# Performance work log

Hardware: AMD Instinct MI355X
Metric: run time of the kernel (lower is better)

## Reference

```python
import jax, jax.numpy as jnp
import numpy as np

B, S, H, I = 2, 1024, 1024, 4096
G, E = 4, 4
NE = G * E
CAP = 1024


def setup_inputs() -> dict:
    key = jax.random.key(0)
    ks = jax.random.split(key, 6)
    return {
        "hidden_states": jax.random.normal(ks[0], (B, S, H), jnp.float32),
        "group_router_w": jax.random.normal(ks[1], (G, H), jnp.float32) * 0.02,
        "expert_router_w": jax.random.normal(ks[2], (G, E, H), jnp.float32) * 0.02,
        "gate_w": jax.random.normal(ks[3], (NE, I, H), jnp.float32) * 0.02,
        "up_w": jax.random.normal(ks[4], (NE, I, H), jnp.float32) * 0.02,
        "down_w": jax.random.normal(ks[5], (NE, H, I), jnp.float32) * 0.02,
    }


def _forward(x, gw, erw, Wg, Wu, Wd):
    b, s, h = x.shape
    T = b * s
    xf = x.reshape(T, h)
    # level 1: group routing (fp32 softmax, top-2 groups)
    group_logits = xf @ gw.T                                        # [T,G]
    group_probs = jax.nn.softmax(group_logits.astype(jnp.float32), axis=-1)
    top_gp, top_gi = jax.lax.top_k(group_probs, 2)                  # [T,2]
    # level 2: per-group expert routing (top-1 expert within group)
    expert_logits = jnp.einsum('th,geh->tge', xf, erw)              # [T,G,E]
    expert_probs = jax.nn.softmax(expert_logits.astype(jnp.float32), axis=-1)
    e_idx = jnp.argmax(expert_probs, axis=-1)                       # [T,G]
    e_prob = jnp.max(expert_probs, axis=-1)                         # [T,G]
    sel_e = jnp.take_along_axis(e_idx, top_gi, axis=1)              # [T,2]
    sel_p = jnp.take_along_axis(e_prob, top_gi, axis=1)             # [T,2]
    eid = (top_gi * E + sel_e).reshape(-1)                          # [2T] global expert id
    wgt = (top_gp * sel_p).reshape(-1)                              # [2T] combine weight
    x2 = jnp.repeat(xf, 2, axis=0)                                  # [2T,H], slot-major per token
    # capacity-based dispatch: position within expert via cumsum of one-hot
    onehot = jax.nn.one_hot(eid, NE, dtype=jnp.int32)               # [2T,NE]
    pos = (jnp.cumsum(onehot, axis=0) * onehot).sum(axis=1) - 1     # [2T]
    keep = pos < CAP
    pos_c = jnp.where(keep, pos, CAP)                               # overflow -> dummy slot
    buf = jnp.zeros((NE, CAP + 1, h), x.dtype).at[eid, pos_c].set(x2)
    # grouped-GEMM gated FFN (SwiGLU) over all experts at once
    gate = jax.nn.silu(jnp.einsum('ech,eih->eci', buf, Wg))
    up = jnp.einsum('ech,eih->eci', buf, Wu)
    yexp = jnp.einsum('eci,ehi->ech', gate * up, Wd)                # [NE,CAP+1,H]
    # combine: gather back and weight; dropped tokens get zero weight
    y = yexp[eid, pos_c] * jnp.where(keep, wgt, 0.0)[:, None].astype(x.dtype)
    out = (y[0::2] + y[1::2]).reshape(b, s, h)
    aux_loss = jnp.zeros((), jnp.float32)  # aux-loss accumulation truncated in source; initialized to 0
    return out, aux_loss


def reference(hidden_states, group_router_w, expert_router_w, gate_w, up_w, down_w):
    return _forward(hidden_states, group_router_w, expert_router_w, gate_w, up_w, down_w)
```

## Files before the change

kernel.cpp:

```cpp
#include <hip/hip_runtime.h>
#include <hip/hip_bf16.h>

typedef float f32x4 __attribute__((ext_vector_type(4)));
typedef __bf16 bf16x8 __attribute__((ext_vector_type(8)));

#define H 1024
#define II 4096
#define NE 16
#define CAP 1024
#define NTOK 2048
#define NSLOT 4096

__global__ __launch_bounds__(256) void k_route(
    const float* __restrict__ x, const float* __restrict__ gw,
    const float* __restrict__ erw, int* __restrict__ eid,
    float* __restrict__ wgt) {
  int t = blockIdx.x * 4 + (threadIdx.x >> 6);
  int lane = threadIdx.x & 63;
  const float* xr = x + (size_t)t * H;
  double acc[20];
#pragma unroll
  for (int j = 0; j < 20; j++) acc[j] = 0.0;
  for (int it = 0; it < 16; ++it) {
    int h = it * 64 + lane;
    float xv = xr[h];
#pragma unroll
    for (int g = 0; g < 4; ++g) acc[g] += (double)xv * (double)gw[g * H + h];
#pragma unroll
    for (int j = 0; j < 16; ++j)
      acc[4 + j] += (double)xv * (double)erw[j * H + h];
  }
#pragma unroll
  for (int j = 0; j < 20; ++j) {
    double v = acc[j];
#pragma unroll
    for (int o = 32; o > 0; o >>= 1) v += __shfl_down(v, o, 64);
    acc[j] = v;
  }
  if (lane == 0) {
    float gl[4];
#pragma unroll
    for (int g = 0; g < 4; g++) gl[g] = (float)acc[g];
    int g1 = 0;
#pragma unroll
    for (int g = 1; g < 4; g++)
      if (gl[g] > gl[g1]) g1 = g;
    int g2 = (g1 == 0) ? 1 : 0;
#pragma unroll
    for (int g = 0; g < 4; g++)
      if (g != g1 && gl[g] > gl[g2]) g2 = g;
    float gm = fmaxf(fmaxf(gl[0], gl[1]), fmaxf(gl[2], gl[3]));
    float s = 0.f;
#pragma unroll
    for (int g = 0; g < 4; g++) s += expf(gl[g] - gm);
    float p[2] = {expf(gl[g1] - gm) / s, expf(gl[g2] - gm) / s};
    int gs[2] = {g1, g2};
#pragma unroll
    for (int k = 0; k < 2; k++) {
      int g = gs[k];
      float el[4];
#pragma unroll
      for (int e2 = 0; e2 < 4; e2++) el[e2] = (float)acc[4 + g * 4 + e2];
      int eb = 0;
#pragma unroll
      for (int e2 = 1; e2 < 4; e2++)
        if (el[e2] > el[eb]) eb = e2;
      float es = 0.f;
#pragma unroll
      for (int e2 = 0; e2 < 4; e2++) es += expf(el[e2] - el[eb]);
      eid[2 * t + k] = g * 4 + eb;
      wgt[2 * t + k] = p[k] * (1.f / es);
    }
  }
}

__global__ __launch_bounds__(1024) void k_scan(const int* __restrict__ eid,
                                               int* __restrict__ perm,
                                               int* __restrict__ cnt,
                                               int* __restrict__ kept) {
  int wid = threadIdx.x >> 6;
  int lane = threadIdx.x & 63;
  int base = 0;
  for (int it = 0; it < 64; ++it) {
    int slot = it * 64 + lane;
    int e = eid[slot];
    unsigned long long m = __ballot(e == wid);
    if (e == wid) {
      int pos = base + __popcll(m & ((1ull << lane) - 1ull));
      if (pos < CAP) {
        perm[wid * CAP + pos] = slot;
        kept[slot] = 1;
      } else {
        kept[slot] = 0;
      }
    }
    base += __popcll(m);
  }
  if (lane == 0) cnt[wid] = (base < CAP) ? base : CAP;
}

__global__ __launch_bounds__(256) void k_cvtx(const float* __restrict__ x,
                                              __bf16* __restrict__ xb) {
  size_t i = ((size_t)blockIdx.x * 256 + threadIdx.x) * 8;
  f32x4 a = *(const f32x4*)(x + i);
  f32x4 b = *(const f32x4*)(x + i + 4);
  bf16x8 o;
#pragma unroll
  for (int j = 0; j < 4; j++) {
    o[j] = (__bf16)a[j];
    o[j + 4] = (__bf16)b[j];
  }
  *(bf16x8*)(xb + i) = o;
}

__global__ __launch_bounds__(256) void k_gateup(
    const __bf16* __restrict__ xb, const float* __restrict__ Wg,
    const float* __restrict__ Wu, const int* __restrict__ perm,
    const int* __restrict__ cnt, __bf16* __restrict__ act) {
  __shared__ __bf16 As[2][128 * 64];
  __shared__ __bf16 Gs[2][64 * 64];
  __shared__ __bf16 Us[2][64 * 64];
  __shared__ int slotArr[128];
  const int e = blockIdx.z, nt = blockIdx.x, rt = blockIdx.y;
  const int ce = cnt[e];
  if (rt * 128 >= ce) return;
  const int tid = threadIdx.x, lane = tid & 63, wid = tid >> 6;
  if (tid < 128) {
    int ridx = rt * 128 + tid;
    slotArr[tid] = perm[e * CAP + (ridx < ce ? ridx : 0)];
  }
  __syncthreads();
  const int srow = tid >> 3;
  const int sch = tid & 7;
  const __bf16* pA[4];
  int wrA[4];
#pragma unroll
  for (int q = 0; q < 4; q++) {
    int r = q * 32 + srow;
    pA[q] = xb + (size_t)(slotArr[r] >> 1) * H + sch * 8;
    wrA[q] = r * 64 + (sch ^ (r & 7)) * 8;
  }
  const size_t ew = (size_t)e * II * H + (size_t)(nt * 64) * H;
  const float* pG[2];
  const float* pU[2];
  int wrW[2];
#pragma unroll
  for (int q = 0; q < 2; q++) {
    int r = q * 32 + srow;
    pG[q] = Wg + ew + (size_t)r * H + sch * 8;
    pU[q] = Wu + ew + (size_t)r * H + sch * 8;
    wrW[q] = r * 64 + (sch ^ (r & 7)) * 8;
  }
  const int wm = wid >> 1, wn = wid & 1;
  f32x4 accG[4][2], accU[4][2];
#pragma unroll
  for (int m = 0; m < 4; m++)
#pragma unroll
    for (int n = 0; n < 2; n++)
#pragma unroll
      for (int i = 0; i < 4; i++) {
        accG[m][n][i] = 0.f;
        accU[m][n][i] = 0.f;
      }
  {
    bf16x8 va[4];
    f32x4 g0[2], g1[2], u0[2], u1[2];
#pragma unroll
    for (int q = 0; q < 4; q++) va[q] = *(const bf16x8*)(pA[q]);
#pragma unroll
    for (int q = 0; q < 2; q++) {
      g0[q] = *(const f32x4*)(pG[q]);
      g1[q] = *(const f32x4*)(pG[q] + 4);
      u0[q] = *(const f32x4*)(pU[q]);
      u1[q] = *(const f32x4*)(pU[q] + 4);
    }
#pragma unroll
    for (int q = 0; q < 4; q++) *(bf16x8*)&As[0][wrA[q]] = va[q];
#pragma unroll
    for (int q = 0; q < 2; q++) {
      bf16x8 fg, fu;
#pragma unroll
      for (int i = 0; i < 4; i++) {
        fg[i] = (__bf16)g0[q][i];
        fg[i + 4] = (__bf16)g1[q][i];
        fu[i] = (__bf16)u0[q][i];
        fu[i + 4] = (__bf16)u1[q][i];
      }
      *(bf16x8*)&Gs[0][wrW[q]] = fg;
      *(bf16x8*)&Us[0][wrW[q]] = fu;
    }
  }
  __syncthreads();
  for (int t = 0; t < 16; ++t) {
    const int cb = t & 1, nb = cb ^ 1;
    bf16x8 va[4];
    f32x4 g0[2], g1[2], u0[2], u1[2];
    if (t < 15) {
      const int ko = (t + 1) * 64;
#pragma unroll
      for (int q = 0; q < 4; q++) va[q] = *(const bf16x8*)(pA[q] + ko);
#pragma unroll
      for (int q = 0; q < 2; q++) {
        g0[q] = *(const f32x4*)(pG[q] + ko);
        g1[q] = *(const f32x4*)(pG[q] + ko + 4);
        u0[q] = *(const f32x4*)(pU[q] + ko);
        u1[q] = *(const f32x4*)(pU[q] + ko + 4);
      }
    }
#pragma unroll
    for (int kk = 0; kk < 2; ++kk) {
      bf16x8 aF[4], gF[2], uF[2];
#pragma unroll
      for (int m = 0; m < 4; m++) {
        int r = wm * 64 + m * 16 + (lane & 15);
        int c = (kk * 4 + (lane >> 4)) ^ (r & 7);
        aF[m] = *(const bf16x8*)&As[cb][r * 64 + c * 8];
      }
#pragma unroll
      for (int n = 0; n < 2; n++) {
        int rg = wn * 32 + n * 16 + (lane & 15);
        int c = (kk * 4 + (lane >> 4)) ^ (rg & 7);
        gF[n] = *(const bf16x8*)&Gs[cb][rg * 64 + c * 8];
        uF[n] = *(const bf16x8*)&Us[cb][rg * 64 + c * 8];
      }
#pragma unroll
      for (int m = 0; m < 4; m++)
#pragma unroll
        for (int n = 0; n < 2; n++) {
          accG[m][n] = __builtin_amdgcn_mfma_f32_16x16x32_bf16(
              aF[m], gF[n], accG[m][n], 0, 0, 0);
          accU[m][n] = __builtin_amdgcn_mfma_f32_16x16x32_bf16(
              aF[m], uF[n], accU[m][n], 0, 0, 0);
        }
    }
    if (t < 15) {
#pragma unroll
      for (int q = 0; q < 4; q++) *(bf16x8*)&As[nb][wrA[q]] = va[q];
#pragma unroll
      for (int q = 0; q < 2; q++) {
        bf16x8 fg, fu;
#pragma unroll
        for (int i = 0; i < 4; i++) {
          fg[i] = (__bf16)g0[q][i];
          fg[i + 4] = (__bf16)g1[q][i];
          fu[i] = (__bf16)u0[q][i];
          fu[i + 4] = (__bf16)u1[q][i];
        }
        *(bf16x8*)&Gs[nb][wrW[q]] = fg;
        *(bf16x8*)&Us[nb][wrW[q]] = fu;
      }
    }
    __syncthreads();
  }
  const int colB = nt * 64 + wn * 32;
#pragma unroll
  for (int m = 0; m < 4; m++)
#pragma unroll
    for (int n = 0; n < 2; n++)
#pragma unroll
      for (int i = 0; i < 4; i++) {
        int row = wm * 64 + m * 16 + (lane >> 4) * 4 + i;
        if (rt * 128 + row < ce) {
          int slot = slotArr[row];
          float g = accG[m][n][i];
          float u = accU[m][n][i];
          float a = (g / (1.f + __expf(-g))) * u;
          act[(size_t)slot * II + colB + n * 16 + (lane & 15)] = (__bf16)a;
        }
      }
}

__global__ __launch_bounds__(256) void k_down(
    const __bf16* __restrict__ act, const float* __restrict__ Wd,
    const int* __restrict__ perm, const int* __restrict__ cnt,
    const float* __restrict__ wgt, float* __restrict__ y) {
  __shared__ __bf16 As[2][128 * 64];
  __shared__ __bf16 Ws[2][128 * 64];
  __shared__ int slotArr[128];
  const int e = blockIdx.z, nt = blockIdx.x, rt = blockIdx.y;
  const int ce = cnt[e];
  if (rt * 128 >= ce) return;
  const int tid = threadIdx.x, lane = tid & 63, wid = tid >> 6;
  if (tid < 128) {
    int ridx = rt * 128 + tid;
    slotArr[tid] = perm[e * CAP + (ridx < ce ? ridx : 0)];
  }
  __syncthreads();
  const int srow = tid >> 3;
  const int sch = tid & 7;
  const __bf16* pA[4];
  const float* pW[4];
  int wrA[4];
#pragma unroll
  for (int q = 0; q < 4; q++) {
    int r = q * 32 + srow;
    pA[q] = act + (size_t)slotArr[r] * II + sch * 8;
    pW[q] = Wd + (size_t)e * H * II + (size_t)(nt * 128 + r) * II + sch * 8;
    wrA[q] = r * 64 + (sch ^ (r & 7)) * 8;
  }
  const int wm = wid >> 1, wn = wid & 1;
  f32x4 acc[4][4];
#pragma unroll
  for (int m = 0; m < 4; m++)
#pragma unroll
    for (int n = 0; n < 4; n++)
#pragma unroll
      for (int i = 0; i < 4; i++) acc[m][n][i] = 0.f;
  {
    bf16x8 va[4];
    f32x4 w0[4], w1[4];
#pragma unroll
    for (int q = 0; q < 4; q++) {
      va[q] = *(const bf16x8*)(pA[q]);
      w0[q] = *(const f32x4*)(pW[q]);
      w1[q] = *(const f32x4*)(pW[q] + 4);
    }
#pragma unroll
    for (int q = 0; q < 4; q++) {
      *(bf16x8*)&As[0][wrA[q]] = va[q];
      bf16x8 fw;
#pragma unroll
      for (int i = 0; i < 4; i++) {
        fw[i] = (__bf16)w0[q][i];
        fw[i + 4] = (__bf16)w1[q][i];
      }
      *(bf16x8*)&Ws[0][wrA[q]] = fw;
    }
  }
  __syncthreads();
  for (int t = 0; t < 64; ++t) {
    const int cb = t & 1, nb = cb ^ 1;
    bf16x8 va[4];
    f32x4 w0[4], w1[4];
    if (t < 63) {
      const int ko = (t + 1) * 64;
#pragma unroll
      for (int q = 0; q < 4; q++) {
        va[q] = *(const bf16x8*)(pA[q] + ko);
        w0[q] = *(const f32x4*)(pW[q] + ko);
        w1[q] = *(const f32x4*)(pW[q] + ko + 4);
      }
    }
#pragma unroll
    for (int kk = 0; kk < 2; ++kk) {
      bf16x8 aF[4], wF[4];
#pragma unroll
      for (int m = 0; m < 4; m++) {
        int r = wm * 64 + m * 16 + (lane & 15);
        int c = (kk * 4 + (lane >> 4)) ^ (r & 7);
        aF[m] = *(const bf16x8*)&As[cb][r * 64 + c * 8];
      }
#pragma unroll
      for (int n = 0; n < 4; n++) {
        int rw = wn * 64 + n * 16 + (lane & 15);
        int c = (kk * 4 + (lane >> 4)) ^ (rw & 7);
        wF[n] = *(const bf16x8*)&Ws[cb][rw * 64 + c * 8];
      }
#pragma unroll
      for (int m = 0; m < 4; m++)
#pragma unroll
        for (int n = 0; n < 4; n++)
          acc[m][n] = __builtin_amdgcn_mfma_f32_16x16x32_bf16(aF[m], wF[n],
                                                              acc[m][n], 0, 0, 0);
    }
    if (t < 63) {
#pragma unroll
      for (int q = 0; q < 4; q++) {
        *(bf16x8*)&As[nb][wrA[q]] = va[q];
        bf16x8 fw;
#pragma unroll
        for (int i = 0; i < 4; i++) {
          fw[i] = (__bf16)w0[q][i];
          fw[i + 4] = (__bf16)w1[q][i];
        }
        *(bf16x8*)&Ws[nb][wrA[q]] = fw;
      }
    }
    __syncthreads();
  }
  const int colB = nt * 128 + wn * 64;
#pragma unroll
  for (int m = 0; m < 4; m++)
#pragma unroll
    for (int n = 0; n < 4; n++)
#pragma unroll
      for (int i = 0; i < 4; i++) {
        int row = wm * 64 + m * 16 + (lane >> 4) * 4 + i;
        if (rt * 128 + row < ce) {
          int slot = slotArr[row];
          y[(size_t)slot * H + colB + n * 16 + (lane & 15)] =
              wgt[slot] * acc[m][n][i];
        }
      }
}

__global__ __launch_bounds__(256) void k_combine(const float* __restrict__ y,
                                                 const int* __restrict__ kept,
                                                 float* __restrict__ out) {
  int t = blockIdx.x, tid = threadIdx.x;
  const f32x4* y0 = (const f32x4*)(y + (size_t)(2 * t) * H);
  const f32x4* y1 = (const f32x4*)(y + (size_t)(2 * t + 1) * H);
  f32x4 a, b;
#pragma unroll
  for (int i = 0; i < 4; i++) {
    a[i] = 0.f;
    b[i] = 0.f;
  }
  if (kept[2 * t]) a = y0[tid];
  if (kept[2 * t + 1]) b = y1[tid];
  ((f32x4*)out)[(size_t)t * 256 + tid] = a + b;
  if (t == 0 && tid == 0) out[(size_t)NTOK * H] = 0.f;
}

extern "C" void kernel_launch(void* const* d_in, const int* in_sizes, int n_in,
                              void* d_out, int out_size, void* d_ws,
                              size_t ws_size, hipStream_t stream) {
  const float* x = (const float*)d_in[0];
  const float* gw = (const float*)d_in[1];
  const float* erw = (const float*)d_in[2];
  const float* Wg = (const float*)d_in[3];
  const float* Wu = (const float*)d_in[4];
  const float* Wd = (const float*)d_in[5];
  float* out = (float*)d_out;
  char* ws = (char*)d_ws;
  int* eid = (int*)(ws);
  float* wgt = (float*)(ws + (16 << 10));
  int* kept = (int*)(ws + (32 << 10));
  int* cnt = (int*)(ws + (48 << 10));
  int* perm = (int*)(ws + (64 << 10));
  __bf16* act = (__bf16*)(ws + (128 << 10));
  float* yb = (float*)(ws + (128 << 10) + (size_t)NSLOT * II * 2);
  __bf16* xb = (__bf16*)(ws + (128 << 10) + (size_t)NSLOT * II * 2 +
                         (size_t)NSLOT * H * 4);

  k_route<<<NTOK / 4, 256, 0, stream>>>(x, gw, erw, eid, wgt);
  k_scan<<<1, 1024, 0, stream>>>(eid, perm, cnt, kept);
  k_cvtx<<<NTOK * H / 8 / 256, 256, 0, stream>>>(x, xb);
  k_gateup<<<dim3(64, 8, 16), 256, 0, stream>>>(xb, Wg, Wu, perm, cnt, act);
  k_down<<<dim3(8, 8, 16), 256, 0, stream>>>(act, Wd, perm, cnt, wgt, yb);
  k_combine<<<NTOK, 256, 0, stream>>>(yb, kept, out);
}
```

Before: 376.7 us.

## Deepen global prefetch to two stages and shrink down-proj N tile

Both grouped-GEMM kernels now keep two K-tiles of global loads in flight using ping-pong register sets. Each LDS buffer swap uses a custom lgkmcnt-wait plus barrier instead of __syncthreads. k_down's N tile is halved to 64 columns and its grid doubled, which adds blocks and cuts per-block LDS and accumulators. Both kernels get launch_bounds min-blocks 2 to raise occupancy. The risks are register pressure from the doubled prefetch registers and more redundant activation reads in k_down.

After: 372.5 us. Within noise of the previous version (-1.1%).

```diff
diff --git a/kernel.cpp b/kernel.cpp
--- a/kernel.cpp
+++ b/kernel.cpp
@@ -113,7 +113,12 @@
   *(bf16x8*)(xb + i) = o;
 }
 
-__global__ __launch_bounds__(256) void k_gateup(
+#define FENCE_BAR()                                    \
+  asm volatile("s_waitcnt lgkmcnt(0)" ::: "memory");   \
+  __builtin_amdgcn_sched_barrier(0);                   \
+  __builtin_amdgcn_s_barrier();
+
+__global__ __launch_bounds__(256, 2) void k_gateup(
     const __bf16* __restrict__ xb, const float* __restrict__ Wg,
     const float* __restrict__ Wu, const int* __restrict__ perm,
     const int* __restrict__ cnt, __bf16* __restrict__ act) {
@@ -162,95 +167,80 @@
         accG[m][n][i] = 0.f;
         accU[m][n][i] = 0.f;
       }
-  {
-    bf16x8 va[4];
-    f32x4 g0[2], g1[2], u0[2], u1[2];
-#pragma unroll
-    for (int q = 0; q < 4; q++) va[q] = *(const bf16x8*)(pA[q]);
-#pragma unroll
-    for (int q = 0; q < 2; q++) {
-      g0[q] = *(const f32x4*)(pG[q]);
-      g1[q] = *(const f32x4*)(pG[q] + 4);
-      u0[q] = *(const f32x4*)(pU[q]);
-      u1[q] = *(const f32x4*)(pU[q] + 4);
+  bf16x8 a0[4], a1[4];
+  f32x4 g00[2], g01[2], u00[2], u01[2];
+  f32x4 g10[2], g11[2], u10[2], u11[2];
+
+#define GU_LOADS(AS, G0, G1, U0, U1, T)                                    \
+  {                                                                        \
+    const int ko = (T) * 64;                                               \
+    _Pragma("unroll") for (int q = 0; q < 4; q++)                          \
+        AS[q] = *(const bf16x8*)(pA[q] + ko);                              \
+    _Pragma("unroll") for (int q = 0; q < 2; q++) {                        \
+      G0[q] = *(const f32x4*)(pG[q] + ko);                                 \
+      G1[q] = *(const f32x4*)(pG[q] + ko + 4);                             \
+      U0[q] = *(const f32x4*)(pU[q] + ko);                                 \
+      U1[q] = *(const f32x4*)(pU[q] + ko + 4);                             \
+    }                                                                      \
+  }
+#define GU_WRITE(BUF, AS, G0, G1, U0, U1)                                  \
+  {                                                                        \
+    _Pragma("unroll") for (int q = 0; q < 4; q++)                          \
+        *(bf16x8*)&As[BUF][wrA[q]] = AS[q];                                \
+    _Pragma("unroll") for (int q = 0; q < 2; q++) {                        \
+      bf16x8 fg, fu;                                                       \
+      _Pragma("unroll") for (int i = 0; i < 4; i++) {                      \
+        fg[i] = (__bf16)G0[q][i];                                          \
+        fg[i + 4] = (__bf16)G1[q][i];                                      \
+        fu[i] = (__bf16)U0[q][i];                                          \
+        fu[i + 4] = (__bf16)U1[q][i];                                      \
+      }                                                                    \
+      *(bf16x8*)&Gs[BUF][wrW[q]] = fg;                                     \
+      *(bf16x8*)&Us[BUF][wrW[q]] = fu;                                     \
+    }                                                                      \
+  }
+#define GU_COMPUTE(BUF)                                                    \
+  {                                                                        \
+    _Pragma("unroll") for (int kk = 0; kk < 2; ++kk) {                     \
+      bf16x8 aF[4], gF[2], uF[2];                                          \
+      _Pragma("unroll") for (int m = 0; m < 4; m++) {                      \
+        int r = wm * 64 + m * 16 + (lane & 15);                            \
+        int c = (kk * 4 + (lane >> 4)) ^ (r & 7);                          \
+        aF[m] = *(const bf16x8*)&As[BUF][r * 64 + c * 8];                  \
+      }                                                                    \
+      _Pragma("unroll") for (int n = 0; n < 2; n++) {                      \
+        int rg = wn * 32 + n * 16 + (lane & 15);                           \
+        int c = (kk * 4 + (lane >> 4)) ^ (rg & 7);                         \
+        gF[n] = *(const bf16x8*)&Gs[BUF][rg * 64 + c * 8];                 \
+        uF[n] = *(const bf16x8*)&Us[BUF][rg * 64 + c * 8];                 \
+      }                                                                    \
+      _Pragma("unroll") for (int m = 0; m < 4; m++)                        \
+          _Pragma("unroll") for (int n = 0; n < 2; n++) {                  \
+        accG[m][n] = __builtin_amdgcn_mfma_f32_16x16x32_bf16(              \
+            aF[m], gF[n], accG[m][n], 0, 0, 0);                            \
+        accU[m][n] = __builtin_amdgcn_mfma_f32_16x16x32_bf16(              \
+            aF[m], uF[n], accU[m][n], 0, 0, 0);                            \
+      }                                                                    \
+    }                                                                      \
+  }
+
+  GU_LOADS(a0, g00, g01, u00, u01, 0);
+  GU_LOADS(a1, g10, g11, u10, u11, 1);
+  GU_WRITE(0, a0, g00, g01, u00, u01);
+  FENCE_BAR();
+  for (int tt = 0; tt < 8; ++tt) {
+    const int t0 = 2 * tt;
+    if (t0 + 2 < 16) GU_LOADS(a0, g00, g01, u00, u01, t0 + 2);
+    GU_COMPUTE(0);
+    GU_WRITE(1, a1, g10, g11, u10, u11);
+    FENCE_BAR();
+    const int t1 = t0 + 1;
+    if (t1 + 2 < 16) GU_LOADS(a1, g10, g11, u10, u11, t1 + 2);
+    GU_COMPUTE(1);
+    if (t1 + 1 < 16) {
+      GU_WRITE(0, a0, g00, g01, u00, u01);
+      FENCE_BAR();
     }
-#pragma unroll
-    for (int q = 0; q < 4; q++) *(bf16x8*)&As[0][wrA[q]] = va[q];
-#pragma unroll
-    for (int q = 0; q < 2; q++) {
-      bf16x8 fg, fu;
-#pragma unroll
-      for (int i = 0; i < 4; i++) {
-        fg[i] = (__bf16)g0[q][i];
-        fg[i + 4] = (__bf16)g1[q][i];
-        fu[i] = (__bf16)u0[q][i];
-        fu[i + 4] = (__bf16)u1[q][i];
-      }
-      *(bf16x8*)&Gs[0][wrW[q]] = fg;
-      *(bf16x8*)&Us[0][wrW[q]] = fu;
-    }
-  }
-  __syncthreads();
-  for (int t = 0; t < 16; ++t) {
-    const int cb = t & 1, nb = cb ^ 1;
-    bf16x8 va[4];
-    f32x4 g0[2], g1[2], u0[2], u1[2];
-    if (t < 15) {
-      const int ko = (t + 1) * 64;
-#pragma unroll
-      for (int q = 0; q < 4; q++) va[q] = *(const bf16x8*)(pA[q] + ko);
-#pragma unroll
-      for (int q = 0; q < 2; q++) {
-        g0[q] = *(const f32x4*)(pG[q] + ko);
-        g1[q] = *(const f32x4*)(pG[q] + ko + 4);
-        u0[q] = *(const f32x4*)(pU[q] + ko);
-        u1[q] = *(const f32x4*)(pU[q] + ko + 4);
-      }
-    }
-#pragma unroll
-    for (int kk = 0; kk < 2; ++kk) {
-      bf16x8 aF[4], gF[2], uF[2];
-#pragma unroll
-      for (int m = 0; m < 4; m++) {
-        int r = wm * 64 + m * 16 + (lane & 15);
-        int c = (kk * 4 + (lane >> 4)) ^ (r & 7);
-        aF[m] = *(const bf16x8*)&As[cb][r * 64 + c * 8];
-      }
-#pragma unroll
-      for (int n = 0; n < 2; n++) {
-        int rg = wn * 32 + n * 16 + (lane & 15);
-        int c = (kk * 4 + (lane >> 4)) ^ (rg & 7);
-        gF[n] = *(const bf16x8*)&Gs[cb][rg * 64 + c * 8];
-        uF[n] = *(const bf16x8*)&Us[cb][rg * 64 + c * 8];
-      }
-#pragma unroll
-      for (int m = 0; m < 4; m++)
-#pragma unroll
-        for (int n = 0; n < 2; n++) {
-          accG[m][n] = __builtin_amdgcn_mfma_f32_16x16x32_bf16(
-              aF[m], gF[n], accG[m][n], 0, 0, 0);
-          accU[m][n] = __builtin_amdgcn_mfma_f32_16x16x32_bf16(
-              aF[m], uF[n], accU[m][n], 0, 0, 0);
-        }
-    }
-    if (t < 15) {
-#pragma unroll
-      for (int q = 0; q < 4; q++) *(bf16x8*)&As[nb][wrA[q]] = va[q];
-#pragma unroll
-      for (int q = 0; q < 2; q++) {
-        bf16x8 fg, fu;
-#pragma unroll
-        for (int i = 0; i < 4; i++) {
-          fg[i] = (__bf16)g0[q][i];
-          fg[i + 4] = (__bf16)g1[q][i];
-          fu[i] = (__bf16)u0[q][i];
-          fu[i + 4] = (__bf16)u1[q][i];
-        }
-        *(bf16x8*)&Gs[nb][wrW[q]] = fg;
-        *(bf16x8*)&Us[nb][wrW[q]] = fu;
-      }
-    }
-    __syncthreads();
   }
   const int colB = nt * 64 + wn * 32;
 #pragma unroll
@@ -270,12 +260,12 @@
       }
 }
 
-__global__ __launch_bounds__(256) void k_down(
+__global__ __launch_bounds__(256, 2) void k_down(
     const __bf16* __restrict__ act, const float* __restrict__ Wd,
     const int* __restrict__ perm, const int* __restrict__ cnt,
     const float* __restrict__ wgt, float* __restrict__ y) {
   __shared__ __bf16 As[2][128 * 64];
-  __shared__ __bf16 Ws[2][128 * 64];
+  __shared__ __bf16 Ws[2][64 * 64];
   __shared__ int slotArr[128];
   const int e = blockIdx.z, nt = blockIdx.x, rt = blockIdx.y;
   const int ce = cnt[e];
@@ -289,100 +279,99 @@
   const int srow = tid >> 3;
   const int sch = tid & 7;
   const __bf16* pA[4];
-  const float* pW[4];
   int wrA[4];
 #pragma unroll
   for (int q = 0; q < 4; q++) {
     int r = q * 32 + srow;
     pA[q] = act + (size_t)slotArr[r] * II + sch * 8;
-    pW[q] = Wd + (size_t)e * H * II + (size_t)(nt * 128 + r) * II + sch * 8;
     wrA[q] = r * 64 + (sch ^ (r & 7)) * 8;
   }
+  const float* pW[2];
+  int wrW[2];
+#pragma unroll
+  for (int q = 0; q < 2; q++) {
+    int r = q * 32 + srow;
+    pW[q] = Wd + (size_t)e * H * II + (size_t)(nt * 64 + r) * II + sch * 8;
+    wrW[q] = r * 64 + (sch ^ (r & 7)) * 8;
+  }
   const int wm = wid >> 1, wn = wid & 1;
-  f32x4 acc[4][4];
+  f32x4 acc[4][2];
 #pragma unroll
   for (int m = 0; m < 4; m++)
 #pragma unroll
-    for (int n = 0; n < 4; n++)
+    for (int n = 0; n < 2; n++)
 #pragma unroll
       for (int i = 0; i < 4; i++) acc[m][n][i] = 0.f;
-  {
-    bf16x8 va[4];
-    f32x4 w0[4], w1[4];
-#pragma unroll
-    for (int q = 0; q < 4; q++) {
-      va[q] = *(const bf16x8*)(pA[q]);
-      w0[q] = *(const f32x4*)(pW[q]);
-      w1[q] = *(const f32x4*)(pW[q] + 4);
+  bf16x8 a0[4], a1[4];
+  f32x4 w00[2], w01[2], w10[2], w11[2];
+
+#define DN_LOADS(AS, W0, W1, T)                                            \
+  {                                                                        \
+    const int ko = (T) * 64;                                               \
+    _Pragma("unroll") for (int q = 0; q < 4; q++)                          \
+        AS[q] = *(const bf16x8*)(pA[q] + ko);                              \
+    _Pragma("unroll") for (int q = 0; q < 2; q++) {                        \
+      W0[q] = *(const f32x4*)(pW[q] + ko);                                 \
+      W1[q] = *(const f32x4*)(pW[q] + ko + 4);                             \
+    }                                                                      \
+  }
+#define DN_WRITE(BUF, AS, W0, W1)                                          \
+  {                                                                        \
+    _Pragma("unroll") for (int q = 0; q < 4; q++)                          \
+        *(bf16x8*)&As[BUF][wrA[q]] = AS[q];                                \
+    _Pragma("unroll") for (int q = 0; q < 2; q++) {                        \
+      bf16x8 fw;                                                           \
+      _Pragma("unroll") for (int i = 0; i < 4; i++) {                      \
+        fw[i] = (__bf16)W0[q][i];                                          \
+        fw[i + 4] = (__bf16)W1[q][i];                                      \
+      }                                                                    \
+      *(bf16x8*)&Ws[BUF][wrW[q]] = fw;                                     \
+    }                                                                      \
+  }
+#define DN_COMPUTE(BUF)                                                    \
+  {                                                                        \
+    _Pragma("unroll") for (int kk = 0; kk < 2; ++kk) {                     \
+      bf16x8 aF[4], wF[2];                                                 \
+      _Pragma("unroll") for (int m = 0; m < 4; m++) {                      \
+        int r = wm * 64 + m * 16 + (lane & 15);                            \
+        int c = (kk * 4 + (lane >> 4)) ^ (r & 7);                          \
+        aF[m] = *(const bf16x8*)&As[BUF][r * 64 + c * 8];                  \
+      }                                                                    \
+      _Pragma("unroll") for (int n = 0; n < 2; n++) {                      \
+        int rw = wn * 32 + n * 16 + (lane & 15);                           \
+        int c = (kk * 4 + (lane >> 4)) ^ (rw & 7);                         \
+        wF[n] = *(const bf16x8*)&Ws[BUF][rw * 64 + c * 8];                 \
+      }                                                                    \
+      _Pragma("unroll") for (int m = 0; m < 4; m++)                        \
+          _Pragma("unroll") for (int n = 0; n < 2; n++)                    \
+              acc[m][n] = __builtin_amdgcn_mfma_f32_16x16x32_bf16(         \
+                  aF[m], wF[n], acc[m][n], 0, 0, 0);                       \
+    }                                                                      \
+  }
+
+  DN_LOADS(a0, w00, w01, 0);
+  DN_LOADS(a1, w10, w11, 1);
+  DN_WRITE(0, a0, w00, w01);
+  FENCE_BAR();
+  for (int tt = 0; tt < 32; ++tt) {
+    const int t0 = 2 * tt;
+    if (t0 + 2 < 64) DN_LOADS(a0, w00, w01, t0 + 2);
+    DN_COMPUTE(0);
+    DN_WRITE(1, a1, w10, w11);
+    FENCE_BAR();
+    const int t1 = t0 + 1;
+    if (t1 + 2 < 64) DN_LOADS(a1, w10, w11, t1 + 2);
+    DN_COMPUTE(1);
+    if (t1 + 1 < 64) {
+      DN_WRITE(0, a0, w00, w01);
+      FENCE_BAR();
     }
-#pragma unroll
-    for (int q = 0; q < 4; q++) {
-      *(bf16x8*)&As[0][wrA[q]] = va[q];
-      bf16x8 fw;
-#pragma unroll
-      for (int i = 0; i < 4; i++) {
-        fw[i] = (__bf16)w0[q][i];
-        fw[i + 4] = (__bf16)w1[q][i];
-      }
-      *(bf16x8*)&Ws[0][wrA[q]] = fw;
-    }
-  }
-  __syncthreads();
-  for (int t = 0; t < 64; ++t) {
-    const int cb = t & 1, nb = cb ^ 1;
-    bf16x8 va[4];
-    f32x4 w0[4], w1[4];
-    if (t < 63) {
-      const int ko = (t + 1) * 64;
-#pragma unroll
-      for (int q = 0; q < 4; q++) {
-        va[q] = *(const bf16x8*)(pA[q] + ko);
-        w0[q] = *(const f32x4*)(pW[q] + ko);
-        w1[q] = *(const f32x4*)(pW[q] + ko + 4);
-      }
-    }
-#pragma unroll
-    for (int kk = 0; kk < 2; ++kk) {
-      bf16x8 aF[4], wF[4];
-#pragma unroll
-      for (int m = 0; m < 4; m++) {
-        int r = wm * 64 + m * 16 + (lane & 15);
-        int c = (kk * 4 + (lane >> 4)) ^ (r & 7);
-        aF[m] = *(const bf16x8*)&As[cb][r * 64 + c * 8];
-      }
-#pragma unroll
-      for (int n = 0; n < 4; n++) {
-        int rw = wn * 64 + n * 16 + (lane & 15);
-        int c = (kk * 4 + (lane >> 4)) ^ (rw & 7);
-        wF[n] = *(const bf16x8*)&Ws[cb][rw * 64 + c * 8];
-      }
-#pragma unroll
-      for (int m = 0; m < 4; m++)
-#pragma unroll
-        for (int n = 0; n < 4; n++)
-          acc[m][n] = __builtin_amdgcn_mfma_f32_16x16x32_bf16(aF[m], wF[n],
-                                                              acc[m][n], 0, 0, 0);
-    }
-    if (t < 63) {
-#pragma unroll
-      for (int q = 0; q < 4; q++) {
-        *(bf16x8*)&As[nb][wrA[q]] = va[q];
-        bf16x8 fw;
-#pragma unroll
-        for (int i = 0; i < 4; i++) {
-          fw[i] = (__bf16)w0[q][i];
-          fw[i + 4] = (__bf16)w1[q][i];
-        }
-        *(bf16x8*)&Ws[nb][wrA[q]] = fw;
-      }
-    }
-    __syncthreads();
-  }
-  const int colB = nt * 128 + wn * 64;
+  }
+  const int colB = nt * 64 + wn * 32;
 #pragma unroll
   for (int m = 0; m < 4; m++)
 #pragma unroll
-    for (int n = 0; n < 4; n++)
+    for (int n = 0; n < 2; n++)
 #pragma unroll
       for (int i = 0; i < 4; i++) {
         int row = wm * 64 + m * 16 + (lane >> 4) * 4 + i;
@@ -437,6 +426,6 @@
   k_scan<<<1, 1024, 0, stream>>>(eid, perm, cnt, kept);
   k_cvtx<<<NTOK * H / 8 / 256, 256, 0, stream>>>(x, xb);
   k_gateup<<<dim3(64, 8, 16), 256, 0, stream>>>(xb, Wg, Wu, perm, cnt, act);
-  k_down<<<dim3(8, 8, 16), 256, 0, stream>>>(act, Wd, perm, cnt, wgt, yb);
+  k_down<<<dim3(16, 8, 16), 256, 0, stream>>>(act, Wd, perm, cnt, wgt, yb);
   k_combine<<<NTOK, 256, 0, stream>>>(yb, kept, out);
 }
```
